# Kernel tuning notes

Measured on AMD Instinct MI355X. Metric: run time of the kernel, lower is better.

Reference implementation:

```python
import jax, jax.numpy as jnp
import numpy as np

BACKBONE_C = 480
NUM_SEG = 4
HIDDEN = 128
IN_DIM = 2 + BACKBONE_C + NUM_SEG + 2  # 488
N_NODES = 200000
N_EDGES = 800000
FH = FW = 128


def _bilinear_sample(feat, vertices, image_size):
    # feat: (C, H, W); vertices: (N, 2) in pixel space.
    # Matches F.grid_sample(..., mode='bilinear', align_corners=True) with
    # grid = vertices/image_size*2 - 1  =>  ix = vx/image_size*(W-1).
    C, H, W = feat.shape
    ix = vertices[:, 0] / image_size * (W - 1)
    iy = vertices[:, 1] / image_size * (H - 1)
    x0 = jnp.floor(ix)
    y0 = jnp.floor(iy)
    wx = ix - x0
    wy = iy - y0
    x0i = jnp.clip(x0.astype(jnp.int32), 0, W - 1)
    x1i = jnp.clip(x0i + 1, 0, W - 1)
    y0i = jnp.clip(y0.astype(jnp.int32), 0, H - 1)
    y1i = jnp.clip(y0i + 1, 0, H - 1)
    f00 = feat[:, y0i, x0i]  # (C, N)
    f01 = feat[:, y0i, x1i]
    f10 = feat[:, y1i, x0i]
    f11 = feat[:, y1i, x1i]
    out = (f00 * (1 - wx) * (1 - wy) + f01 * wx * (1 - wy)
           + f10 * (1 - wx) * wy + f11 * wx * wy)
    return out.T  # (N, C)


def setup_inputs() -> dict:
    key = jax.random.key(0)
    k = jax.random.split(key, 8)
    vertices = jax.random.uniform(k[0], (N_NODES, 2), jnp.float32) * 512.0
    backbone_features = jax.random.normal(k[1], (1, BACKBONE_C, FH, FW), jnp.float32)
    seg_probs = jax.random.uniform(k[2], (1, NUM_SEG, FH, FW), jnp.float32)
    edge_index = jax.random.randint(k[3], (2, N_EDGES), 0, N_NODES, jnp.int64)
    s1 = 1.0 / np.sqrt(IN_DIM)
    s2 = 1.0 / np.sqrt(HIDDEN)
    W1 = jax.random.uniform(k[4], (HIDDEN, IN_DIM), jnp.float32, -s1, s1)
    b1 = jax.random.uniform(k[5], (HIDDEN,), jnp.float32, -s1, s1)
    W2 = jax.random.uniform(k[6], (HIDDEN, HIDDEN), jnp.float32, -s2, s2)
    b2 = jax.random.uniform(k[7], (HIDDEN,), jnp.float32, -s2, s2)
    return {"vertices": vertices, "backbone_features": backbone_features,
            "seg_probs": seg_probs, "edge_index": edge_index,
            "W1": W1, "b1": b1, "W2": W2, "b2": b2, "image_size": 512}


def reference(vertices, backbone_features, seg_probs, edge_index, W1, b1, W2, b2, image_size):
    N = vertices.shape[0]
    coords_norm = vertices / image_size  # (N, 2)
    backbone_feats = _bilinear_sample(backbone_features[0], vertices, image_size)  # (N, C)
    seg_stats = _bilinear_sample(seg_probs[0], vertices, image_size)  # (N, num_seg)
    # degree via scatter-add over both endpoints
    idx = jnp.concatenate([edge_index[0], edge_index[1]]).astype(jnp.int32)
    degree = jax.ops.segment_sum(jnp.ones(idx.shape[0], jnp.float32), idx, num_segments=N)
    degree_norm = degree / (degree.max() + 1e-6)
    # distance to nearest image boundary, normalized by image_size/2
    dx = jnp.minimum(vertices[:, 0], image_size - vertices[:, 0])
    dy = jnp.minimum(vertices[:, 1], image_size - vertices[:, 1])
    dist_to_boundary = jnp.minimum(dx, dy) / (image_size / 2)
    structural = jnp.stack([degree_norm, dist_to_boundary], axis=1)  # (N, 2)
    node_feats = jnp.concatenate([coords_norm, backbone_feats, seg_stats, structural], axis=1)  # (N, 488)
    h = jax.nn.relu(node_feats @ W1.T + b1)
    h = jax.nn.relu(h @ W2.T + b2)
    return h
```

## Files before the change

kernel.cpp:

```cpp
#include <hip/hip_runtime.h>

typedef _Float16 half_t;
typedef __attribute__((ext_vector_type(2))) _Float16 halfx2;
typedef __attribute__((ext_vector_type(8))) _Float16 halfx8;
typedef __attribute__((ext_vector_type(4))) float floatx4;

#define N_NODES 200000
#define N_EDGES 800000
#define NPOS    16384
#define KIN     484

#define NSLICE  32
#define NRANGE  8
#define RNODES  25000
#define RWORDS  6250
#define CWORDS  50000
#define SCHUNK  12500

#define KT_TRANS 4096
#define KT_HISTO (KT_TRANS + NSLICE * NRANGE)
#define KT_W1F   (KT_HISTO + 8)
#define KT_GRID  (KT_W1F + 1)

#define WS_DEGPK 0
#define WS_DEG   6400000
#define WS_MAXD  7200000
#define WS_W2F   7200064
#define WS_W1F   7232832
#define WS_U     7363904
#define WS_BT    11558208

__global__ __launch_bounds__(256) void kT(const float* __restrict__ bb,
                                          const float* __restrict__ seg,
                                          const int* __restrict__ e,
                                          const float* __restrict__ W1,
                                          const float* __restrict__ W2,
                                          unsigned* __restrict__ degpk,
                                          half_t* __restrict__ Bt,
                                          half_t* __restrict__ w1f,
                                          half_t* __restrict__ w2f,
                                          unsigned* __restrict__ maxd) {
  __shared__ __align__(16) char sm[25600];

  const int tid = threadIdx.x;
  const int bid = blockIdx.x;
  const int wave = tid >> 6, lane = tid & 63;
  const int l15 = lane & 15, q4 = lane >> 4;

  if (bid < KT_TRANS) {
    const int pt = bid >> 4, kt = bid & 15;
    const int p0 = pt * 64, kb = kt * 32;
    const int kw = kb + wave * 8;
    halfx8 h;
    for (int i = 0; i < 8; ++i) {
      int k = kw + i;
      float v = 0.f;
      if (k < 480)      v = bb[(long)k * NPOS + p0 + lane];
      else if (k < KIN) v = seg[(long)(k - 480) * NPOS + p0 + lane];
      h[i] = (half_t)v;
    }
    *(halfx8*)&Bt[(long)(p0 + lane) * 512 + kw] = h;
  } else if (bid < KT_HISTO) {
    unsigned* cnt = (unsigned*)sm;
    const int hb = bid - KT_TRANS;
    const int s  = hb >> 3;
    const int r  = hb & 7;
    const int lo = r * RNODES;

    for (int i = tid; i < 64 + RWORDS; i += 256) cnt[i] = 0;
    __syncthreads();

#define HBIN(v) { unsigned d = (unsigned)(v) - (unsigned)lo;                 \
                  bool ok = d < (unsigned)RNODES;                            \
                  unsigned w = ok ? (d >> 2) + 64u : (unsigned)lane;         \
                  unsigned a_ = ok ? (1u << ((d & 3u) << 3)) : 0u;           \
                  atomicAdd(&cnt[w], a_); }

    const int4* E4 = (const int4*)e + s * SCHUNK;
    for (int base = 0; base < 12288; base += 1024) {
      int4 a = E4[base + tid];
      int4 b = E4[base + tid + 256];
      int4 c = E4[base + tid + 512];
      int4 d4 = E4[base + tid + 768];
      HBIN(a.x); HBIN(a.y); HBIN(a.z); HBIN(a.w);
      HBIN(b.x); HBIN(b.y); HBIN(b.z); HBIN(b.w);
      HBIN(c.x); HBIN(c.y); HBIN(c.z); HBIN(c.w);
      HBIN(d4.x); HBIN(d4.y); HBIN(d4.z); HBIN(d4.w);
    }
    if (tid < SCHUNK - 12288) {
      int4 a = E4[12288 + tid];
      HBIN(a.x); HBIN(a.y); HBIN(a.z); HBIN(a.w);
    }
#undef HBIN
    __syncthreads();

    unsigned* dst = degpk + s * CWORDS + r * RWORDS;
    for (int i = tid; i < RWORDS; i += 256) dst[i] = cnt[64 + i];
  } else if (bid < KT_W1F) {
    const int t = bid - KT_HISTO;
    const int j = t * 16 + l15;
    for (int c = 0; c < 4; ++c) {
      int kbi = c * 4 + wave;
      halfx8 h;
      for (int i = 0; i < 8; ++i) {
        int k = kbi * 32 + q4 * 8 + i;
        h[i] = (half_t)((k < KIN) ? W1[j * 488 + 2 + k] : 0.f);
      }
      *(halfx8*)&w1f[(t * 16 + kbi) * 512 + lane * 8] = h;
    }
  } else {
    if (tid == 0) *maxd = 0u;
    for (int i = tid; i < 128 * 128; i += 256) {
      int k8   = i & 7;
      int il15 = (i >> 3) & 15;
      int iq4  = (i >> 7) & 3;
      int ks32 = (i >> 9) & 1;
      int hh   = (i >> 10) & 1;
      int t    = i >> 11;
      int row = t * 16 + il15;
      int col = hh * 64 + ks32 * 32 + iq4 * 8 + k8;
      w2f[i] = (half_t)W2[row * 128 + col];
    }
  }
}

__global__ __launch_bounds__(256) void k1(const half_t* __restrict__ Bt,
                                          const half_t* __restrict__ w1f,
                                          half_t* __restrict__ U) {
  __shared__ half_t Ol[64 * 136];

  const int tid = threadIdx.x, bid = blockIdx.x;
  const int wave = tid >> 6, lane = tid & 63;
  const int l15 = lane & 15, q4 = lane >> 4;
  const int n0 = bid * 64;

  floatx4 acc[8];
  for (int t = 0; t < 8; ++t) acc[t] = (floatx4){0.f, 0.f, 0.f, 0.f};

  const half_t* bt = Bt + (long)(n0 + wave * 16 + l15) * 512 + q4 * 8;
  for (int kbi = 0; kbi < 16; ++kbi) {
    halfx8 af = *(const halfx8*)&bt[kbi * 32];
    for (int t = 0; t < 8; ++t) {
      halfx8 bf = *(const halfx8*)&w1f[(t * 16 + kbi) * 512 + lane * 8];
      acc[t] = __builtin_amdgcn_mfma_f32_16x16x32_f16(af, bf, acc[t], 0, 0, 0);
    }
  }

  for (int t = 0; t < 8; ++t)
    for (int r = 0; r < 4; ++r)
      Ol[(wave * 16 + q4 * 4 + r) * 136 + t * 16 + l15] = (half_t)acc[t][r];
  __syncthreads();
  for (int it = 0; it < 4; ++it) {
    int idx = tid + it * 256;
    int n = idx >> 4, c8 = (idx & 15) * 8;
    *(halfx8*)(U + (long)(n0 + n) * 128 + c8) = *(const halfx8*)&Ol[n * 136 + c8];
  }
}

__global__ __launch_bounds__(256) void k2(const unsigned* __restrict__ degpk,
                                          unsigned* __restrict__ deg,
                                          unsigned* __restrict__ maxd) {
  const int w4 = blockIdx.x * 256 + threadIdx.x;
  unsigned m = 0;
  if (w4 < CWORDS / 4) {
    uint4 s = make_uint4(0u, 0u, 0u, 0u);
    for (int c = 0; c < NSLICE; ++c) {
      uint4 v = *(const uint4*)&degpk[c * CWORDS + w4 * 4];
      s.x += v.x; s.y += v.y; s.z += v.z; s.w += v.w;
    }
    unsigned words[4] = {s.x, s.y, s.z, s.w};
    for (int k = 0; k < 4; ++k) {
      unsigned sw = words[k];
      uint4 o = make_uint4(sw & 255u, (sw >> 8) & 255u,
                           (sw >> 16) & 255u, sw >> 24);
      *(uint4*)&deg[w4 * 16 + k * 4] = o;
      m = max(m, max(max(o.x, o.y), max(o.z, o.w)));
    }
  }
  for (int off = 32; off > 0; off >>= 1) {
    unsigned o = (unsigned)__shfl_down((int)m, off);
    m = max(m, o);
  }
  if ((threadIdx.x & 63) == 0) atomicMax(maxd, m);
}

__global__ __launch_bounds__(256, 8) void k_main(const float* __restrict__ vertices,
                                              const float* __restrict__ W1,
                                              const float* __restrict__ b1,
                                              const float* __restrict__ b2,
                                              const unsigned* __restrict__ deg,
                                              const unsigned* __restrict__ maxd,
                                              const half_t* __restrict__ U,
                                              const half_t* __restrict__ w2f,
                                              float* __restrict__ out) {
  __shared__ half_t At[64 * 136];
  __shared__ int   pPos[64];
  __shared__ float pW[4][64];
  __shared__ float pE[4][64];
  __shared__ float b2l[128];

  const int tid = threadIdx.x;
  const int nodeBase = blockIdx.x * 64;

  if (tid < 128) b2l[tid] = b2[tid];

  if (tid < 64) {
    int n = nodeBase + tid;
    float vx = vertices[2 * n], vy = vertices[2 * n + 1];
    float ix = vx * (127.0f / 512.0f), iy = vy * (127.0f / 512.0f);
    float fx = floorf(ix), fy = floorf(iy);
    float wx = ix - fx, wy = iy - fy;
    int x0 = min(max((int)fx, 0), 127);
    int y0 = min(max((int)fy, 0), 127);
    pPos[tid] = y0 * 128 + x0;
    pW[0][tid] = (1.f - wx) * (1.f - wy);
    pW[1][tid] = wx * (1.f - wy);
    pW[2][tid] = (1.f - wx) * wy;
    pW[3][tid] = wx * wy;
    pE[0][tid] = vx * (1.f / 512.f);
    pE[1][tid] = vy * (1.f / 512.f);
    float md = (float)(*maxd) + 1e-6f;
    pE[2][tid] = (float)deg[n] / md;
    float dx = fminf(vx, 512.f - vx), dy = fminf(vy, 512.f - vy);
    pE[3][tid] = fminf(dx, dy) * (1.f / 256.f);
  }

  const int jp = tid & 63, q = tid >> 6;
  const int j2 = jp * 2;
  const float* r0 = W1 + j2 * 488;
  const float* r1 = r0 + 488;
  float c00 = r0[0], c01 = r0[1], c06 = r0[486], c07 = r0[487];
  float c10 = r1[0], c11 = r1[1], c16 = r1[486], c17 = r1[487];
  float bb0 = b1[j2], bb1 = b1[j2 + 1];
  __syncthreads();

#pragma unroll 4
  for (int it = 0; it < 16; ++it) {
    int ln = it * 4 + q;
    int pos = pPos[ln];
    float w00 = pW[0][ln], w01 = pW[1][ln], w10 = pW[2][ln], w11 = pW[3][ln];
    float cx = pE[0][ln], cy = pE[1][ln], dn = pE[2][ln], db = pE[3][ln];
    const half_t* base = U + (long)pos * 128 + j2;
    halfx2 u00 = *(const halfx2*)(base);
    halfx2 u01 = *(const halfx2*)(base + 128);
    halfx2 u10 = *(const halfx2*)(base + 16384);
    halfx2 u11 = *(const halfx2*)(base + 16512);
    float z0 = bb0 + c00 * cx + c01 * cy + c06 * dn + c07 * db
             + w00 * (float)u00.x + w01 * (float)u01.x
             + w10 * (float)u10.x + w11 * (float)u11.x;
    float z1 = bb1 + c10 * cx + c11 * cy + c16 * dn + c17 * db
             + w00 * (float)u00.y + w01 * (float)u01.y
             + w10 * (float)u10.y + w11 * (float)u11.y;
    halfx2 h;
    h.x = (half_t)fmaxf(z0, 0.f);
    h.y = (half_t)fmaxf(z1, 0.f);
    *(halfx2*)&At[ln * 136 + j2] = h;
  }
  __syncthreads();

  const int wave = tid >> 6, lane = tid & 63;
  const int l15 = lane & 15, q4 = lane >> 4;
  const half_t* wf = w2f + (q4 * 16 + l15) * 8;
  floatx4 acc[8];
  for (int t = 0; t < 8; ++t) acc[t] = (floatx4){0.f, 0.f, 0.f, 0.f};

  for (int h = 0; h < 2; ++h)
    for (int ks32 = 0; ks32 < 2; ++ks32) {
      halfx8 af = *(const halfx8*)&At[(wave * 16 + l15) * 136 + h * 64 +
                                      ks32 * 32 + q4 * 8];
      for (int t = 0; t < 8; ++t) {
        halfx8 bf = *(const halfx8*)&wf[(t * 4 + h * 2 + ks32) * 512];
        acc[t] = __builtin_amdgcn_mfma_f32_16x16x32_f16(af, bf, acc[t], 0, 0, 0);
      }
    }

  for (int t = 0; t < 8; ++t) {
    int col = t * 16 + l15;
    float bias = b2l[col];
    int row0 = nodeBase + wave * 16 + q4 * 4;
    for (int r = 0; r < 4; ++r)
      out[(long)(row0 + r) * 128 + col] = fmaxf(acc[t][r] + bias, 0.f);
  }
}

extern "C" void kernel_launch(void* const* d_in, const int* in_sizes, int n_in,
                              void* d_out, int out_size, void* d_ws, size_t ws_size,
                              hipStream_t stream) {
  const float* vertices = (const float*)d_in[0];
  const float* bb       = (const float*)d_in[1];
  const float* seg      = (const float*)d_in[2];
  const int*   edges    = (const int*)d_in[3];
  const float* W1       = (const float*)d_in[4];
  const float* b1       = (const float*)d_in[5];
  const float* W2       = (const float*)d_in[6];
  const float* b2       = (const float*)d_in[7];

  char* ws = (char*)d_ws;
  unsigned* degpk = (unsigned*)(ws + WS_DEGPK);
  unsigned* deg   = (unsigned*)(ws + WS_DEG);
  unsigned* maxd  = (unsigned*)(ws + WS_MAXD);
  half_t*   w2f   = (half_t*)(ws + WS_W2F);
  half_t*   w1f   = (half_t*)(ws + WS_W1F);
  half_t*   U     = (half_t*)(ws + WS_U);
  half_t*   Bt    = (half_t*)(ws + WS_BT);
  float*    outp  = (float*)d_out;

  kT<<<KT_GRID, 256, 0, stream>>>(bb, seg, edges, W1, W2, degpk, Bt, w1f, w2f, maxd);
  k1<<<256, 256, 0, stream>>>(Bt, w1f, U);
  k2<<<49, 256, 0, stream>>>(degpk, deg, maxd);
  k_main<<<3125, 256, 0, stream>>>(vertices, W1, b1, b2, deg, maxd, U, w2f, outp);
}
```

Baseline: 222.7 us.

## Merge GEMM and degree-reduce kernels, rebalance histogram slicing, precompact W1 edge columns

The separate k1 (feature-grid GEMM) and k2 (degree reduction) kernels are combined into one launch, with extra blocks doing the reduction, which removes a kernel launch and its serialization. The edge histogram now uses 64 slices over 4 node ranges, so each block covers a wider node range with larger LDS counters and fewer edges. It also writes a packed float4 copy of W1's coordinate and structural columns so k_main reads them contiguously instead of striding through W1. The costs are higher LDS use per histogram block (lower occupancy), twice as much partial-count data for the reduce, and a larger workspace.

Measured after the change: 223.8 us. Within noise of the previous version (+0.5%).

```diff
diff --git a/kernel.cpp b/kernel.cpp
--- a/kernel.cpp
+++ b/kernel.cpp
@@ -10,27 +10,28 @@
 #define NPOS    16384
 #define KIN     484
 
-#define NSLICE  32
-#define NRANGE  8
-#define RNODES  25000
-#define RWORDS  6250
+#define NSLICE  64
+#define NRANGE  4
+#define RNODES  50000
+#define RWORDS  12500
 #define CWORDS  50000
-#define SCHUNK  12500
-
-#define KT_TRANS 4096
-#define KT_HISTO (KT_TRANS + NSLICE * NRANGE)
-#define KT_W1F   (KT_HISTO + 8)
-#define KT_GRID  (KT_W1F + 1)
+#define SCHUNK  6250
+
+#define A_TRANS_END 4096
+#define A_HISTO_END (A_TRANS_END + NSLICE * NRANGE)
+#define A_W1F_END   (A_HISTO_END + 8)
+#define A_GRID      (A_W1F_END + 1)
 
 #define WS_DEGPK 0
-#define WS_DEG   6400000
-#define WS_MAXD  7200000
-#define WS_W2F   7200064
-#define WS_W1F   7232832
-#define WS_U     7363904
-#define WS_BT    11558208
-
-__global__ __launch_bounds__(256) void kT(const float* __restrict__ bb,
+#define WS_DEG   12800000
+#define WS_MAXD  13600000
+#define WS_W1C   13600064
+#define WS_W2F   13602112
+#define WS_W1F   13634880
+#define WS_U     13765952
+#define WS_BT    17960256
+
+__global__ __launch_bounds__(256) void kA(const float* __restrict__ bb,
                                           const float* __restrict__ seg,
                                           const int* __restrict__ e,
                                           const float* __restrict__ W1,
@@ -39,15 +40,16 @@
                                           half_t* __restrict__ Bt,
                                           half_t* __restrict__ w1f,
                                           half_t* __restrict__ w2f,
+                                          float4* __restrict__ w1c,
                                           unsigned* __restrict__ maxd) {
-  __shared__ __align__(16) char sm[25600];
+  __shared__ __align__(16) char sm[50432];
 
   const int tid = threadIdx.x;
   const int bid = blockIdx.x;
   const int wave = tid >> 6, lane = tid & 63;
   const int l15 = lane & 15, q4 = lane >> 4;
 
-  if (bid < KT_TRANS) {
+  if (bid < A_TRANS_END) {
     const int pt = bid >> 4, kt = bid & 15;
     const int p0 = pt * 64, kb = kt * 32;
     const int kw = kb + wave * 8;
@@ -60,11 +62,11 @@
       h[i] = (half_t)v;
     }
     *(halfx8*)&Bt[(long)(p0 + lane) * 512 + kw] = h;
-  } else if (bid < KT_HISTO) {
+  } else if (bid < A_HISTO_END) {
     unsigned* cnt = (unsigned*)sm;
-    const int hb = bid - KT_TRANS;
-    const int s  = hb >> 3;
-    const int r  = hb & 7;
+    const int hb = bid - A_TRANS_END;
+    const int s  = hb >> 2;
+    const int r  = hb & 3;
     const int lo = r * RNODES;
 
     for (int i = tid; i < 64 + RWORDS; i += 256) cnt[i] = 0;
@@ -77,7 +79,7 @@
                   atomicAdd(&cnt[w], a_); }
 
     const int4* E4 = (const int4*)e + s * SCHUNK;
-    for (int base = 0; base < 12288; base += 1024) {
+    for (int base = 0; base < 6144; base += 1024) {
       int4 a = E4[base + tid];
       int4 b = E4[base + tid + 256];
       int4 c = E4[base + tid + 512];
@@ -87,8 +89,8 @@
       HBIN(c.x); HBIN(c.y); HBIN(c.z); HBIN(c.w);
       HBIN(d4.x); HBIN(d4.y); HBIN(d4.z); HBIN(d4.w);
     }
-    if (tid < SCHUNK - 12288) {
-      int4 a = E4[12288 + tid];
+    if (tid < SCHUNK - 6144) {
+      int4 a = E4[6144 + tid];
       HBIN(a.x); HBIN(a.y); HBIN(a.z); HBIN(a.w);
     }
 #undef HBIN
@@ -96,8 +98,8 @@
 
     unsigned* dst = degpk + s * CWORDS + r * RWORDS;
     for (int i = tid; i < RWORDS; i += 256) dst[i] = cnt[64 + i];
-  } else if (bid < KT_W1F) {
-    const int t = bid - KT_HISTO;
+  } else if (bid < A_W1F_END) {
+    const int t = bid - A_HISTO_END;
     const int j = t * 16 + l15;
     for (int c = 0; c < 4; ++c) {
       int kbi = c * 4 + wave;
@@ -110,6 +112,10 @@
     }
   } else {
     if (tid == 0) *maxd = 0u;
+    if (tid < 128) {
+      const float* row = W1 + tid * 488;
+      w1c[tid] = make_float4(row[0], row[1], row[486], row[487]);
+    }
     for (int i = tid; i < 128 * 128; i += 256) {
       int k8   = i & 7;
       int il15 = (i >> 3) & 15;
@@ -124,68 +130,70 @@
   }
 }
 
-__global__ __launch_bounds__(256) void k1(const half_t* __restrict__ Bt,
+__global__ __launch_bounds__(256) void kB(const half_t* __restrict__ Bt,
                                           const half_t* __restrict__ w1f,
-                                          half_t* __restrict__ U) {
-  __shared__ half_t Ol[64 * 136];
-
-  const int tid = threadIdx.x, bid = blockIdx.x;
-  const int wave = tid >> 6, lane = tid & 63;
-  const int l15 = lane & 15, q4 = lane >> 4;
-  const int n0 = bid * 64;
-
-  floatx4 acc[8];
-  for (int t = 0; t < 8; ++t) acc[t] = (floatx4){0.f, 0.f, 0.f, 0.f};
-
-  const half_t* bt = Bt + (long)(n0 + wave * 16 + l15) * 512 + q4 * 8;
-  for (int kbi = 0; kbi < 16; ++kbi) {
-    halfx8 af = *(const halfx8*)&bt[kbi * 32];
-    for (int t = 0; t < 8; ++t) {
-      halfx8 bf = *(const halfx8*)&w1f[(t * 16 + kbi) * 512 + lane * 8];
-      acc[t] = __builtin_amdgcn_mfma_f32_16x16x32_f16(af, bf, acc[t], 0, 0, 0);
-    }
-  }
-
-  for (int t = 0; t < 8; ++t)
-    for (int r = 0; r < 4; ++r)
-      Ol[(wave * 16 + q4 * 4 + r) * 136 + t * 16 + l15] = (half_t)acc[t][r];
-  __syncthreads();
-  for (int it = 0; it < 4; ++it) {
-    int idx = tid + it * 256;
-    int n = idx >> 4, c8 = (idx & 15) * 8;
-    *(halfx8*)(U + (long)(n0 + n) * 128 + c8) = *(const halfx8*)&Ol[n * 136 + c8];
-  }
-}
-
-__global__ __launch_bounds__(256) void k2(const unsigned* __restrict__ degpk,
+                                          const unsigned* __restrict__ degpk,
+                                          half_t* __restrict__ U,
                                           unsigned* __restrict__ deg,
                                           unsigned* __restrict__ maxd) {
-  const int w4 = blockIdx.x * 256 + threadIdx.x;
-  unsigned m = 0;
-  if (w4 < CWORDS / 4) {
-    uint4 s = make_uint4(0u, 0u, 0u, 0u);
-    for (int c = 0; c < NSLICE; ++c) {
-      uint4 v = *(const uint4*)&degpk[c * CWORDS + w4 * 4];
-      s.x += v.x; s.y += v.y; s.z += v.z; s.w += v.w;
-    }
-    unsigned words[4] = {s.x, s.y, s.z, s.w};
-    for (int k = 0; k < 4; ++k) {
-      unsigned sw = words[k];
-      uint4 o = make_uint4(sw & 255u, (sw >> 8) & 255u,
-                           (sw >> 16) & 255u, sw >> 24);
-      *(uint4*)&deg[w4 * 16 + k * 4] = o;
-      m = max(m, max(max(o.x, o.y), max(o.z, o.w)));
-    }
-  }
-  for (int off = 32; off > 0; off >>= 1) {
-    unsigned o = (unsigned)__shfl_down((int)m, off);
-    m = max(m, o);
-  }
-  if ((threadIdx.x & 63) == 0) atomicMax(maxd, m);
+  __shared__ half_t Ol[64 * 136];
+
+  const int tid = threadIdx.x, bid = blockIdx.x;
+
+  if (bid < 256) {
+    const int wave = tid >> 6, lane = tid & 63;
+    const int l15 = lane & 15, q4 = lane >> 4;
+    const int n0 = bid * 64;
+
+    floatx4 acc[8];
+    for (int t = 0; t < 8; ++t) acc[t] = (floatx4){0.f, 0.f, 0.f, 0.f};
+
+    const half_t* bt = Bt + (long)(n0 + wave * 16 + l15) * 512 + q4 * 8;
+    for (int kbi = 0; kbi < 16; ++kbi) {
+      halfx8 af = *(const halfx8*)&bt[kbi * 32];
+      for (int t = 0; t < 8; ++t) {
+        halfx8 bf = *(const halfx8*)&w1f[(t * 16 + kbi) * 512 + lane * 8];
+        acc[t] = __builtin_amdgcn_mfma_f32_16x16x32_f16(af, bf, acc[t], 0, 0, 0);
+      }
+    }
+
+    for (int t = 0; t < 8; ++t)
+      for (int r = 0; r < 4; ++r)
+        Ol[(wave * 16 + q4 * 4 + r) * 136 + t * 16 + l15] = (half_t)acc[t][r];
+    __syncthreads();
+    for (int it = 0; it < 4; ++it) {
+      int idx = tid + it * 256;
+      int n = idx >> 4, c8 = (idx & 15) * 8;
+      *(halfx8*)(U + (long)(n0 + n) * 128 + c8) = *(const halfx8*)&Ol[n * 136 + c8];
+    }
+  } else {
+    const int w4 = (bid - 256) * 256 + tid;
+    unsigned m = 0;
+    if (w4 < CWORDS / 4) {
+      uint4 s = make_uint4(0u, 0u, 0u, 0u);
+      for (int c = 0; c < NSLICE; ++c) {
+        uint4 v = *(const uint4*)&degpk[c * CWORDS + w4 * 4];
+        s.x += v.x; s.y += v.y; s.z += v.z; s.w += v.w;
+      }
+      unsigned words[4] = {s.x, s.y, s.z, s.w};
+      for (int k = 0; k < 4; ++k) {
+        unsigned sw = words[k];
+        uint4 o = make_uint4(sw & 255u, (sw >> 8) & 255u,
+                             (sw >> 16) & 255u, sw >> 24);
+        *(uint4*)&deg[w4 * 16 + k * 4] = o;
+        m = max(m, max(max(o.x, o.y), max(o.z, o.w)));
+      }
+    }
+    for (int off = 32; off > 0; off >>= 1) {
+      unsigned o = (unsigned)__shfl_down((int)m, off);
+      m = max(m, o);
+    }
+    if ((tid & 63) == 0) atomicMax(maxd, m);
+  }
 }
 
 __global__ __launch_bounds__(256, 8) void k_main(const float* __restrict__ vertices,
-                                              const float* __restrict__ W1,
+                                              const float4* __restrict__ w1c,
                                               const float* __restrict__ b1,
                                               const float* __restrict__ b2,
                                               const unsigned* __restrict__ deg,
@@ -227,10 +235,9 @@
 
   const int jp = tid & 63, q = tid >> 6;
   const int j2 = jp * 2;
-  const float* r0 = W1 + j2 * 488;
-  const float* r1 = r0 + 488;
-  float c00 = r0[0], c01 = r0[1], c06 = r0[486], c07 = r0[487];
-  float c10 = r1[0], c11 = r1[1], c16 = r1[486], c17 = r1[487];
+  float4 cA = w1c[j2], cB = w1c[j2 + 1];
+  float c00 = cA.x, c01 = cA.y, c06 = cA.z, c07 = cA.w;
+  float c10 = cB.x, c11 = cB.y, c16 = cB.z, c17 = cB.w;
   float bb0 = b1[j2], bb1 = b1[j2 + 1];
   __syncthreads();
 
@@ -299,14 +306,15 @@
   unsigned* degpk = (unsigned*)(ws + WS_DEGPK);
   unsigned* deg   = (unsigned*)(ws + WS_DEG);
   unsigned* maxd  = (unsigned*)(ws + WS_MAXD);
+  float4*   w1c   = (float4*)(ws + WS_W1C);
   half_t*   w2f   = (half_t*)(ws + WS_W2F);
   half_t*   w1f   = (half_t*)(ws + WS_W1F);
   half_t*   U     = (half_t*)(ws + WS_U);
   half_t*   Bt    = (half_t*)(ws + WS_BT);
   float*    outp  = (float*)d_out;
 
-  kT<<<KT_GRID, 256, 0, stream>>>(bb, seg, edges, W1, W2, degpk, Bt, w1f, w2f, maxd);
-  k1<<<256, 256, 0, stream>>>(Bt, w1f, U);
-  k2<<<49, 256, 0, stream>>>(degpk, deg, maxd);
-  k_main<<<3125, 256, 0, stream>>>(vertices, W1, b1, b2, deg, maxd, U, w2f, outp);
+  kA<<<A_GRID, 256, 0, stream>>>(bb, seg, edges, W1, W2, degpk, Bt, w1f, w2f,
+                                 w1c, maxd);
+  kB<<<256 + 49, 256, 0, stream>>>(Bt, w1f, degpk, U, deg, maxd);
+  k_main<<<3125, 256, 0, stream>>>(vertices, w1c, b1, b2, deg, maxd, U, w2f, outp);
 }
```

## Fuse feature-map transpose into the W1 projection GEMM and split weight prep

Applied to the files above, without the earlier changes.

The separate pass that transposed backbone and segmentation maps into a half-precision Bt buffer is removed. The projection GEMM now loads fp32 feature rows directly, converts them and stages them through per-wave LDS before the MFMA, and runs in the same launch as the degree histogram. Weight packing moves to a small kernel that also precomputes the four per-row W1 coefficients, so k_main reads one float4 instead of strided W1 rows. This avoids the Bt global write and read round trip, but leaves the W1 GEMM blocks with a global-to-LDS conversion in the inner loop and one extra launch.

Measured after the change: 209.0 us, median of 2. 6.2% less time.

```diff
diff --git a/kernel.cpp b/kernel.cpp
--- a/kernel.cpp
+++ b/kernel.cpp
@@ -17,52 +17,118 @@
 #define CWORDS  50000
 #define SCHUNK  12500
 
-#define KT_TRANS 4096
-#define KT_HISTO (KT_TRANS + NSLICE * NRANGE)
-#define KT_W1F   (KT_HISTO + 8)
-#define KT_GRID  (KT_W1F + 1)
-
 #define WS_DEGPK 0
 #define WS_DEG   6400000
 #define WS_MAXD  7200000
-#define WS_W2F   7200064
-#define WS_W1F   7232832
-#define WS_U     7363904
-#define WS_BT    11558208
-
-__global__ __launch_bounds__(256) void kT(const float* __restrict__ bb,
+#define WS_W1C   7200064
+#define WS_W2F   7202112
+#define WS_W1F   7234880
+#define WS_U     7365952
+
+__global__ __launch_bounds__(256) void k0(const float* __restrict__ W1,
+                                          const float* __restrict__ W2,
+                                          half_t* __restrict__ w2f,
+                                          half_t* __restrict__ w1f,
+                                          float4* __restrict__ w1c,
+                                          unsigned* __restrict__ maxd) {
+  const int tid = threadIdx.x, bid = blockIdx.x;
+  const int wave = tid >> 6, lane = tid & 63;
+  const int l15 = lane & 15, q4 = lane >> 4;
+
+  if (bid == 0) {
+    if (tid == 0) *maxd = 0u;
+    if (tid < 128) {
+      const float* row = W1 + tid * 488;
+      w1c[tid] = make_float4(row[0], row[1], row[486], row[487]);
+    }
+    for (int i = tid; i < 128 * 128; i += 256) {
+      int k8   = i & 7;
+      int il15 = (i >> 3) & 15;
+      int iq4  = (i >> 7) & 3;
+      int ks32 = (i >> 9) & 1;
+      int hh   = (i >> 10) & 1;
+      int t    = i >> 11;
+      int row = t * 16 + il15;
+      int col = hh * 64 + ks32 * 32 + iq4 * 8 + k8;
+      w2f[i] = (half_t)W2[row * 128 + col];
+    }
+  } else {
+    const int t = bid - 1;
+    const int j = t * 16 + l15;
+    for (int c = 0; c < 4; ++c) {
+      int kbi = c * 4 + wave;
+      halfx8 h;
+      for (int i = 0; i < 8; ++i) {
+        int k = kbi * 32 + q4 * 8 + i;
+        h[i] = (half_t)((k < KIN) ? W1[j * 488 + 2 + k] : 0.f);
+      }
+      *(halfx8*)&w1f[(t * 16 + kbi) * 512 + lane * 8] = h;
+    }
+  }
+}
+
+__global__ __launch_bounds__(256) void k1(const float* __restrict__ bb,
                                           const float* __restrict__ seg,
                                           const int* __restrict__ e,
-                                          const float* __restrict__ W1,
-                                          const float* __restrict__ W2,
+                                          const half_t* __restrict__ w1f,
                                           unsigned* __restrict__ degpk,
-                                          half_t* __restrict__ Bt,
-                                          half_t* __restrict__ w1f,
-                                          half_t* __restrict__ w2f,
-                                          unsigned* __restrict__ maxd) {
+                                          half_t* __restrict__ U) {
   __shared__ __align__(16) char sm[25600];
 
-  const int tid = threadIdx.x;
-  const int bid = blockIdx.x;
+  const int tid = threadIdx.x, bid = blockIdx.x;
   const int wave = tid >> 6, lane = tid & 63;
-  const int l15 = lane & 15, q4 = lane >> 4;
-
-  if (bid < KT_TRANS) {
-    const int pt = bid >> 4, kt = bid & 15;
-    const int p0 = pt * 64, kb = kt * 32;
-    const int kw = kb + wave * 8;
-    halfx8 h;
-    for (int i = 0; i < 8; ++i) {
-      int k = kw + i;
-      float v = 0.f;
-      if (k < 480)      v = bb[(long)k * NPOS + p0 + lane];
-      else if (k < KIN) v = seg[(long)(k - 480) * NPOS + p0 + lane];
-      h[i] = (half_t)v;
-    }
-    *(halfx8*)&Bt[(long)(p0 + lane) * 512 + kw] = h;
-  } else if (bid < KT_HISTO) {
+
+  if (bid < 256) {
+    const int l15 = lane & 15, q4 = lane >> 4;
+    const int kk = lane >> 1, ph = lane & 1;
+    const int n0 = bid * 64;
+    half_t* Ol = (half_t*)sm;
+    half_t* Bp = (half_t*)(sm + 17408) + wave * 640;
+    const int pbase = n0 + wave * 16 + ph * 8;
+
+    floatx4 acc[8];
+    for (int t = 0; t < 8; ++t) acc[t] = (floatx4){0.f, 0.f, 0.f, 0.f};
+
+    for (int kbi = 0; kbi < 16; ++kbi) {
+      const int k = kbi * 32 + kk;
+      float vals[8];
+      if (k < 480) {
+        const float* src = bb + (long)k * NPOS + pbase;
+        float4 a = *(const float4*)src;
+        float4 b4 = *(const float4*)(src + 4);
+        vals[0] = a.x; vals[1] = a.y; vals[2] = a.z; vals[3] = a.w;
+        vals[4] = b4.x; vals[5] = b4.y; vals[6] = b4.z; vals[7] = b4.w;
+      } else if (k < KIN) {
+        const float* src = seg + (long)(k - 480) * NPOS + pbase;
+        float4 a = *(const float4*)src;
+        float4 b4 = *(const float4*)(src + 4);
+        vals[0] = a.x; vals[1] = a.y; vals[2] = a.z; vals[3] = a.w;
+        vals[4] = b4.x; vals[5] = b4.y; vals[6] = b4.z; vals[7] = b4.w;
+      } else {
+        for (int i = 0; i < 8; ++i) vals[i] = 0.f;
+      }
+      for (int i = 0; i < 8; ++i)
+        Bp[(ph * 8 + i) * 40 + kk] = (half_t)vals[i];
+
+      halfx8 af = *(const halfx8*)&Bp[l15 * 40 + q4 * 8];
+      for (int t = 0; t < 8; ++t) {
+        halfx8 bf = *(const halfx8*)&w1f[(t * 16 + kbi) * 512 + lane * 8];
+        acc[t] = __builtin_amdgcn_mfma_f32_16x16x32_f16(af, bf, acc[t], 0, 0, 0);
+      }
+    }
+
+    for (int t = 0; t < 8; ++t)
+      for (int r = 0; r < 4; ++r)
+        Ol[(wave * 16 + q4 * 4 + r) * 136 + t * 16 + l15] = (half_t)acc[t][r];
+    __syncthreads();
+    for (int it = 0; it < 4; ++it) {
+      int idx = tid + it * 256;
+      int n = idx >> 4, c8 = (idx & 15) * 8;
+      *(halfx8*)(U + (long)(n0 + n) * 128 + c8) = *(const halfx8*)&Ol[n * 136 + c8];
+    }
+  } else {
     unsigned* cnt = (unsigned*)sm;
-    const int hb = bid - KT_TRANS;
+    const int hb = bid - 256;
     const int s  = hb >> 3;
     const int r  = hb & 7;
     const int lo = r * RNODES;
@@ -96,64 +162,6 @@
 
     unsigned* dst = degpk + s * CWORDS + r * RWORDS;
     for (int i = tid; i < RWORDS; i += 256) dst[i] = cnt[64 + i];
-  } else if (bid < KT_W1F) {
-    const int t = bid - KT_HISTO;
-    const int j = t * 16 + l15;
-    for (int c = 0; c < 4; ++c) {
-      int kbi = c * 4 + wave;
-      halfx8 h;
-      for (int i = 0; i < 8; ++i) {
-        int k = kbi * 32 + q4 * 8 + i;
-        h[i] = (half_t)((k < KIN) ? W1[j * 488 + 2 + k] : 0.f);
-      }
-      *(halfx8*)&w1f[(t * 16 + kbi) * 512 + lane * 8] = h;
-    }
-  } else {
-    if (tid == 0) *maxd = 0u;
-    for (int i = tid; i < 128 * 128; i += 256) {
-      int k8   = i & 7;
-      int il15 = (i >> 3) & 15;
-      int iq4  = (i >> 7) & 3;
-      int ks32 = (i >> 9) & 1;
-      int hh   = (i >> 10) & 1;
-      int t    = i >> 11;
-      int row = t * 16 + il15;
-      int col = hh * 64 + ks32 * 32 + iq4 * 8 + k8;
-      w2f[i] = (half_t)W2[row * 128 + col];
-    }
-  }
-}
-
-__global__ __launch_bounds__(256) void k1(const half_t* __restrict__ Bt,
-                                          const half_t* __restrict__ w1f,
-                                          half_t* __restrict__ U) {
-  __shared__ half_t Ol[64 * 136];
-
-  const int tid = threadIdx.x, bid = blockIdx.x;
-  const int wave = tid >> 6, lane = tid & 63;
-  const int l15 = lane & 15, q4 = lane >> 4;
-  const int n0 = bid * 64;
-
-  floatx4 acc[8];
-  for (int t = 0; t < 8; ++t) acc[t] = (floatx4){0.f, 0.f, 0.f, 0.f};
-
-  const half_t* bt = Bt + (long)(n0 + wave * 16 + l15) * 512 + q4 * 8;
-  for (int kbi = 0; kbi < 16; ++kbi) {
-    halfx8 af = *(const halfx8*)&bt[kbi * 32];
-    for (int t = 0; t < 8; ++t) {
-      halfx8 bf = *(const halfx8*)&w1f[(t * 16 + kbi) * 512 + lane * 8];
-      acc[t] = __builtin_amdgcn_mfma_f32_16x16x32_f16(af, bf, acc[t], 0, 0, 0);
-    }
-  }
-
-  for (int t = 0; t < 8; ++t)
-    for (int r = 0; r < 4; ++r)
-      Ol[(wave * 16 + q4 * 4 + r) * 136 + t * 16 + l15] = (half_t)acc[t][r];
-  __syncthreads();
-  for (int it = 0; it < 4; ++it) {
-    int idx = tid + it * 256;
-    int n = idx >> 4, c8 = (idx & 15) * 8;
-    *(halfx8*)(U + (long)(n0 + n) * 128 + c8) = *(const halfx8*)&Ol[n * 136 + c8];
   }
 }
 
@@ -185,7 +193,7 @@
 }
 
 __global__ __launch_bounds__(256, 8) void k_main(const float* __restrict__ vertices,
-                                              const float* __restrict__ W1,
+                                              const float4* __restrict__ w1c,
                                               const float* __restrict__ b1,
                                               const float* __restrict__ b2,
                                               const unsigned* __restrict__ deg,
@@ -227,10 +235,9 @@
 
   const int jp = tid & 63, q = tid >> 6;
   const int j2 = jp * 2;
-  const float* r0 = W1 + j2 * 488;
-  const float* r1 = r0 + 488;
-  float c00 = r0[0], c01 = r0[1], c06 = r0[486], c07 = r0[487];
-  float c10 = r1[0], c11 = r1[1], c16 = r1[486], c17 = r1[487];
+  float4 cA = w1c[j2], cB = w1c[j2 + 1];
+  float c00 = cA.x, c01 = cA.y, c06 = cA.z, c07 = cA.w;
+  float c10 = cB.x, c11 = cB.y, c16 = cB.z, c17 = cB.w;
   float bb0 = b1[j2], bb1 = b1[j2 + 1];
   __syncthreads();
 
@@ -299,14 +306,14 @@
   unsigned* degpk = (unsigned*)(ws + WS_DEGPK);
   unsigned* deg   = (unsigned*)(ws + WS_DEG);
   unsigned* maxd  = (unsigned*)(ws + WS_MAXD);
+  float4*   w1c   = (float4*)(ws + WS_W1C);
   half_t*   w2f   = (half_t*)(ws + WS_W2F);
   half_t*   w1f   = (half_t*)(ws + WS_W1F);
   half_t*   U     = (half_t*)(ws + WS_U);
-  half_t*   Bt    = (half_t*)(ws + WS_BT);
   float*    outp  = (float*)d_out;
 
-  kT<<<KT_GRID, 256, 0, stream>>>(bb, seg, edges, W1, W2, degpk, Bt, w1f, w2f, maxd);
-  k1<<<256, 256, 0, stream>>>(Bt, w1f, U);
+  k0<<<9, 256, 0, stream>>>(W1, W2, w2f, w1f, w1c, maxd);
+  k1<<<512, 256, 0, stream>>>(bb, seg, edges, w1f, degpk, U);
   k2<<<49, 256, 0, stream>>>(degpk, deg, maxd);
-  k_main<<<3125, 256, 0, stream>>>(vertices, W1, b1, b2, deg, maxd, U, w2f, outp);
-}
+  k_main<<<3125, 256, 0, stream>>>(vertices, w1c, b1, b2, deg, maxd, U, w2f, outp);
+}
```
